# Kernel optimization log

Measured on AMD Instinct MI355X. Metric: run time of the kernel, lower is better.

The kernel has to match this reference:

```python
import jax, jax.numpy as jnp
import numpy as np
from math import sqrt

V, D, H, HD, L, F, P, NL = 32000, 768, 12, 64, 12, 3072, 2048, 2
B, S = 8, 1024
EPS = 1e-5


def setup_inputs() -> dict:
    key = jax.random.key(0)
    ks = jax.random.split(key, 12)
    n = lambda k, sh: (jax.random.normal(k, sh, jnp.float32) * 0.02)
    return {
        'tokens': jax.random.randint(ks[0], (B, S), 0, V, dtype=jnp.int32),
        'tok_emb': n(ks[1], (V, D)),
        'pos_emb': n(ks[2], (P, D)),
        'emb_ln_s': jnp.ones((D,), jnp.float32), 'emb_ln_b': jnp.zeros((D,), jnp.float32),
        'Wq': n(ks[3], (L, H, D, HD)), 'bq': jnp.zeros((L, H, HD), jnp.float32),
        'Wk': n(ks[4], (L, H, D, HD)), 'bk': jnp.zeros((L, H, HD), jnp.float32),
        'Wv': n(ks[5], (L, H, D, HD)), 'bv': jnp.zeros((L, H, HD), jnp.float32),
        'Wo': n(ks[6], (L, D, D)), 'bo': jnp.zeros((L, D), jnp.float32),
        'ln1_s': jnp.ones((L, D), jnp.float32), 'ln1_b': jnp.zeros((L, D), jnp.float32),
        'ln2_s': jnp.ones((L, D), jnp.float32), 'ln2_b': jnp.zeros((L, D), jnp.float32),
        'W1': n(ks[7], (L, D, F)), 'b1': jnp.zeros((L, F), jnp.float32),
        'W2': n(ks[8], (L, F, D)), 'b2': jnp.zeros((L, D), jnp.float32),
        'Wc': n(ks[9], (D, NL)), 'bc': jnp.zeros((NL,), jnp.float32),
    }


def _ln(x, s, b):
    m = jnp.mean(x, -1, keepdims=True)
    v = jnp.mean((x - m) ** 2, -1, keepdims=True)
    return (x - m) * jax.lax.rsqrt(v + EPS) * s + b


def reference(tokens, tok_emb, pos_emb, emb_ln_s, emb_ln_b,
              Wq, bq, Wk, bk, Wv, bv, Wo, bo,
              ln1_s, ln1_b, ln2_s, ln2_b, W1, b1, W2, b2, Wc, bc):
    b, s = tokens.shape
    # embeddings (dropout is eval-mode identity)
    x = tok_emb[tokens] + pos_emb[:s][None, :, :]          # [b, s, D]
    x = _ln(x, emb_ln_s, emb_ln_b)
    scale = 1.0 / sqrt(HD)
    for l in range(L):
        xn = _ln(x, ln1_s[l], ln1_b[l])
        q = jnp.einsum('bsd,hdk->bhsk', xn, Wq[l]) + bq[l][:, None, :]
        k = jnp.einsum('bsd,hdk->bhsk', xn, Wk[l]) + bk[l][:, None, :]
        v = jnp.einsum('bsd,hdk->bhsk', xn, Wv[l]) + bv[l][:, None, :]
        scores = jnp.einsum('bhsk,bhtk->bhst', q, k) * scale   # [b,H,s,s]
        w = jax.nn.softmax(scores, axis=-1)
        o = jnp.einsum('bhst,bhtk->bhsk', w, v)                # [b,H,s,HD]
        o = o.transpose(0, 2, 1, 3).reshape(b, s, D)           # concat heads
        x = x + o @ Wo[l] + bo[l]
        xn = _ln(x, ln2_s[l], ln2_b[l])
        h = jax.nn.gelu(xn @ W1[l] + b1[l], approximate=False)
        x = x + h @ W2[l] + b2[l]
    # CLS token -> classifier (dropout identity)
    return x[:, 0, :] @ Wc + bc                                # [b, NL]
```

## Files before the change

### kernel.cpp

```cpp
#include <hip/hip_runtime.h>
#include <hip/hip_bf16.h>
#include <math.h>

#define B_   8
#define S_   1024
#define D_   768
#define H_   12
#define HD_  64
#define L_   12
#define F_   3072
#define NTOK 8192

typedef __bf16 bf16x8 __attribute__((ext_vector_type(8)));
typedef float  f32x4  __attribute__((ext_vector_type(4)));
typedef unsigned short u16;

static __device__ __forceinline__ unsigned short f2bf_bits(float f) {
    __hip_bfloat16 h = __float2bfloat16(f);
    return __builtin_bit_cast(unsigned short, h);
}
static __device__ __forceinline__ float bf2f(unsigned short u) {
    unsigned int t = ((unsigned int)u) << 16;
    return __builtin_bit_cast(float, t);
}
static __device__ __forceinline__ void gload16(const void* g, void* l) {
    __builtin_amdgcn_global_load_lds(
        (__attribute__((address_space(1))) void*)g,
        (__attribute__((address_space(3))) void*)l, 16, 0, 0);
}

__global__ __launch_bounds__(256)
void prep_layer_kernel(const float* __restrict__ Wq, const float* __restrict__ Wk,
                       const float* __restrict__ Wv, const float* __restrict__ Wo,
                       const float* __restrict__ W1, const float* __restrict__ W2,
                       int l, __hip_bfloat16* __restrict__ wbuf)
{
    const int id = blockIdx.x;
    const float* src; __hip_bfloat16* dst;
    int R, C, r0, c0;
    if (id < 432) {
        int dtile = id % 12, t = id / 12;
        int which = t / 12, h = t % 12;
        src = (which == 0 ? Wq : which == 1 ? Wk : Wv) + (size_t)(l*12 + h) * 768 * 64;
        dst = wbuf + (size_t)(which*768 + h*64) * 768;
        R = 768; C = 64; r0 = dtile * 64; c0 = 0;
    } else if (id < 576) {
        int t = id - 432;
        src = Wo + (size_t)l * 768 * 768;
        dst = wbuf + 1769472;
        R = 768; C = 768; r0 = (t / 12) * 64; c0 = (t % 12) * 64;
    } else if (id < 1152) {
        int t = id - 576;
        src = W1 + (size_t)l * 768 * 3072;
        dst = wbuf + 2359296;
        R = 768; C = 3072; r0 = (t % 12) * 64; c0 = (t / 12) * 64;
    } else {
        int t = id - 1152;
        src = W2 + (size_t)l * 3072 * 768;
        dst = wbuf + 4718592;
        R = 3072; C = 768; r0 = (t / 12) * 64; c0 = (t % 12) * 64;
    }
    __shared__ u16 T[64][68];
    const int t = threadIdx.x;
    const int row = t >> 2, part = t & 3;
#pragma unroll
    for (int j = 0; j < 4; ++j) {
        const int c4 = (part + j*4) * 4;
        float4 v = *(const float4*)(src + (size_t)(r0 + row) * C + c0 + c4);
        T[c4+0][row] = f2bf_bits(v.x);
        T[c4+1][row] = f2bf_bits(v.y);
        T[c4+2][row] = f2bf_bits(v.z);
        T[c4+3][row] = f2bf_bits(v.w);
    }
    __syncthreads();
    const int c = t >> 2;
    u16* drow = (u16*)dst + (size_t)(c0 + c) * R + r0;
#pragma unroll
    for (int j = 0; j < 4; ++j) {
        const int r4 = (part + j*4) * 4;
        ushort4 pk = *(const ushort4*)&T[c][r4];
        *(ushort4*)(drow + r4) = pk;
    }
}

__global__ __launch_bounds__(256)
void prep_bqkv_kernel(const float* __restrict__ bq, const float* __restrict__ bk,
                      const float* __restrict__ bv, float* __restrict__ bqkv)
{
    int i = blockIdx.x * 256 + threadIdx.x;
    int l = i / 2304, c = i % 2304;
    int which = c / 768, hk = c % 768;
    const float* src = which == 0 ? bq : which == 1 ? bk : bv;
    bqkv[i] = src[l*768 + hk];
}

__global__ __launch_bounds__(256)
void embed_ln_kernel(const int* __restrict__ tokens, const float* __restrict__ tok_emb,
                     const float* __restrict__ pos_emb, const float* __restrict__ gam,
                     const float* __restrict__ bet, float* __restrict__ x)
{
    const int row  = blockIdx.x*4 + (threadIdx.x >> 6);
    const int lane = threadIdx.x & 63;
    const int s    = row & (S_-1);
    const int tok  = tokens[row];
    const float* te = tok_emb + (size_t)tok * D_;
    const float* pe = pos_emb + (size_t)s   * D_;
    float v[12]; float s1 = 0.f, s2 = 0.f;
#pragma unroll
    for (int c = 0; c < 3; ++c) {
        const int base = c*256 + lane*4;
        float4 a = *(const float4*)(te + base);
        float4 p = *(const float4*)(pe + base);
        float t0 = a.x+p.x, t1 = a.y+p.y, t2 = a.z+p.z, t3 = a.w+p.w;
        v[c*4+0]=t0; v[c*4+1]=t1; v[c*4+2]=t2; v[c*4+3]=t3;
        s1 += t0+t1+t2+t3;
        s2 += t0*t0 + t1*t1 + t2*t2 + t3*t3;
    }
#pragma unroll
    for (int off = 32; off > 0; off >>= 1) { s1 += __shfl_xor(s1, off); s2 += __shfl_xor(s2, off); }
    const float mean = s1 * (1.f/768.f);
    const float rstd = rsqrtf(s2*(1.f/768.f) - mean*mean + 1e-5f);
    float* xr = x + (size_t)row * D_;
#pragma unroll
    for (int c = 0; c < 3; ++c) {
        const int base = c*256 + lane*4;
        float4 g = *(const float4*)(gam + base);
        float4 bb = *(const float4*)(bet + base);
        float4 o;
        o.x = (v[c*4+0]-mean)*rstd*g.x + bb.x;
        o.y = (v[c*4+1]-mean)*rstd*g.y + bb.y;
        o.z = (v[c*4+2]-mean)*rstd*g.z + bb.z;
        o.w = (v[c*4+3]-mean)*rstd*g.w + bb.w;
        *(float4*)(xr + base) = o;
    }
}

__global__ __launch_bounds__(256)
void ln_kernel(const float* __restrict__ xin, const float* __restrict__ gam,
               const float* __restrict__ bet, __hip_bfloat16* __restrict__ out)
{
    const int row  = blockIdx.x*4 + (threadIdx.x >> 6);
    const int lane = threadIdx.x & 63;
    const float* xr = xin + (size_t)row * D_;
    float v[12]; float s1 = 0.f, s2 = 0.f;
#pragma unroll
    for (int c = 0; c < 3; ++c) {
        float4 t = *(const float4*)(xr + c*256 + lane*4);
        v[c*4+0]=t.x; v[c*4+1]=t.y; v[c*4+2]=t.z; v[c*4+3]=t.w;
        s1 += t.x+t.y+t.z+t.w;
        s2 += t.x*t.x + t.y*t.y + t.z*t.z + t.w*t.w;
    }
#pragma unroll
    for (int off = 32; off > 0; off >>= 1) { s1 += __shfl_xor(s1, off); s2 += __shfl_xor(s2, off); }
    const float mean = s1 * (1.f/768.f);
    const float rstd = rsqrtf(s2*(1.f/768.f) - mean*mean + 1e-5f);
    unsigned short* op = (unsigned short*)out + (size_t)row * D_;
#pragma unroll
    for (int c = 0; c < 3; ++c) {
        const int base = c*256 + lane*4;
        float4 g = *(const float4*)(gam + base);
        float4 bb = *(const float4*)(bet + base);
        ushort4 pk;
        pk.x = f2bf_bits((v[c*4+0]-mean)*rstd*g.x + bb.x);
        pk.y = f2bf_bits((v[c*4+1]-mean)*rstd*g.y + bb.y);
        pk.z = f2bf_bits((v[c*4+2]-mean)*rstd*g.z + bb.z);
        pk.w = f2bf_bits((v[c*4+3]-mean)*rstd*g.w + bb.w);
        *(ushort4*)(op + base) = pk;
    }
}

template<int EPI>
__global__ __launch_bounds__(256)
void gemm128_kernel(const __hip_bfloat16* __restrict__ A,
                    const __hip_bfloat16* __restrict__ Bt,
                    const float* __restrict__ bias,
                    __hip_bfloat16* __restrict__ outb,
                    __hip_bfloat16* __restrict__ outv,
                    int N, int K, int nTiles)
{
    __shared__ __align__(16) char smem[32768];
    char* const As0 = smem;
    char* const As1 = smem + 8192;
    char* const Bs0 = smem + 16384;
    char* const Bs1 = smem + 24576;

    const int tid  = threadIdx.x;
    const int lane = tid & 63;
    const int wid  = tid >> 6;

    const int nwg   = gridDim.x;
    const int chunk = nwg >> 3;
    const int bid   = blockIdx.x;
    const int swz   = (bid & 7) * chunk + (bid >> 3);
    const int m0 = (swz / nTiles) * 128;
    const int n0 = (swz % nTiles) * 128;

    const int l4 = lane >> 2;
    const int sswz = ((lane & 3) ^ ((l4 >> 1) & 3)) * 8;
    const __hip_bfloat16* aSrc = A  + (size_t)(m0 + wid*32 + l4) * K + sswz;
    const __hip_bfloat16* bSrc = Bt + (size_t)(n0 + wid*32 + l4) * K + sswz;
    const int sOff = wid*2048 + lane*16;

    f32x4 acc[4][4] = {};
    const int wm = wid >> 1, wn = wid & 1;
    const int cl = lane & 15, hi = lane >> 4;

    int aoff[4], boff[4];
#pragma unroll
    for (int m = 0; m < 4; ++m) {
        const int row = wm*64 + m*16 + cl;
        aoff[m] = row*64 + ((hi ^ ((row >> 1) & 3)) << 4);
    }
#pragma unroll
    for (int n = 0; n < 4; ++n) {
        const int row = wn*64 + n*16 + cl;
        boff[n] = row*64 + ((hi ^ ((row >> 1) & 3)) << 4);
    }

#pragma unroll
    for (int i = 0; i < 2; ++i) {
        gload16(aSrc + (size_t)i*16*K, As0 + sOff + i*1024);
        gload16(bSrc + (size_t)i*16*K, Bs0 + sOff + i*1024);
    }

    int buf = 0;
    for (int kt = 0; kt < K; kt += 32, buf ^= 1) {
        __syncthreads();
        if (kt + 32 < K) {
            char* an = buf ? As0 : As1;
            char* bn = buf ? Bs0 : Bs1;
#pragma unroll
            for (int i = 0; i < 2; ++i) {
                gload16(aSrc + kt + 32 + (size_t)i*16*K, an + sOff + i*1024);
                gload16(bSrc + kt + 32 + (size_t)i*16*K, bn + sOff + i*1024);
            }
        }
        const char* ac = buf ? As1 : As0;
        const char* bc = buf ? Bs1 : Bs0;

        bf16x8 af[4], bfr[4];
#pragma unroll
        for (int m = 0; m < 4; ++m) af[m]  = *(const bf16x8*)(ac + aoff[m]);
#pragma unroll
        for (int n = 0; n < 4; ++n) bfr[n] = *(const bf16x8*)(bc + boff[n]);
#pragma unroll
        for (int m = 0; m < 4; ++m)
#pragma unroll
            for (int n = 0; n < 4; ++n)
                acc[m][n] = __builtin_amdgcn_mfma_f32_16x16x32_bf16(af[m], bfr[n], acc[m][n], 0, 0, 0);
    }

    __syncthreads();

    const bool vpath = (EPI == 0) && (n0 >= 1536);

    if (!vpath) {
#pragma unroll
        for (int n = 0; n < 4; ++n) {
            const int col2 = wn*64 + n*16 + cl;
            const float bv = bias[n0 + col2];
#pragma unroll
            for (int m = 0; m < 4; ++m) {
#pragma unroll
                for (int i = 0; i < 4; ++i) {
                    const int row = wm*64 + m*16 + hi*4 + i;
                    float v = acc[m][n][i] + bv;
                    if constexpr (EPI == 1) {
                        const float y = 0.7978845608f * (v + 0.044715f*v*v*v);
                        const float e = __expf(-2.0f * fabsf(y));
                        const float th = (1.0f - e) / (1.0f + e);
                        v = 0.5f * v * (1.0f + copysignf(th, y));
                    }
                    *(u16*)(smem + row*256 + ((((col2 >> 3) ^ (row & 15))) << 4)
                                 + ((col2 & 7) << 1)) = f2bf_bits(v);
                }
            }
        }
        __syncthreads();
        const int strideN = (EPI == 0) ? 1536 : N;
        const int r  = tid >> 1;
        const int cb = tid & 1;
        char* dst = (char*)outb + ((size_t)(m0 + r) * strideN + n0) * 2;
#pragma unroll
        for (int j = 0; j < 8; ++j) {
            const int ch = cb + j*2;
            float4 vv = *(const float4*)(smem + r*256 + ((ch ^ (r & 15)) << 4));
            *(float4*)(dst + ch*16) = vv;
        }
    } else {
#pragma unroll
        for (int n = 0; n < 4; ++n) {
            const int hdl = wn*64 + n*16 + cl;
            const float bv = bias[n0 + hdl];
#pragma unroll
            for (int m = 0; m < 4; ++m) {
                const int sl = wm*64 + m*16 + hi*4;
                ushort4 pk;
                pk.x = f2bf_bits(acc[m][n][0] + bv);
                pk.y = f2bf_bits(acc[m][n][1] + bv);
                pk.z = f2bf_bits(acc[m][n][2] + bv);
                pk.w = f2bf_bits(acc[m][n][3] + bv);
                *(ushort4*)(smem + hdl*256 + ((((sl >> 3) ^ (hdl & 15))) << 4) + (sl & 7)*2) = pk;
            }
        }
        __syncthreads();
        const int hdl2 = tid >> 1;
        const int sh   = (tid & 1) * 64;
        const int hdg  = (n0 - 1536) + hdl2;
        const int bb   = m0 >> 10;
        u16* dst = (u16*)outv + ((size_t)(bb*768) + hdg)*1024 + (m0 & 1023) + sh;
#pragma unroll
        for (int j = 0; j < 8; ++j) {
            const int slot = ((sh >> 3) + j) ^ (hdl2 & 15);
            *(float4*)((char*)dst + j*16) = *(const float4*)(smem + hdl2*256 + (slot << 4));
        }
    }
}

__global__ __launch_bounds__(256)
void gemm_res_kernel(const __hip_bfloat16* __restrict__ A,
                     const __hip_bfloat16* __restrict__ Bt,
                     const float* __restrict__ bias,
                     float* __restrict__ outf,
                     int N, int K, int nTiles)
{
    __shared__ __align__(16) char smem[49152];
    char* const As0 = smem;
    char* const As1 = smem + 8192;
    char* const Bs0 = smem + 16384;
    char* const Bs1 = smem + 32768;

    const int tid  = threadIdx.x;
    const int lane = tid & 63;
    const int wid  = tid >> 6;

    const int nwg   = gridDim.x;
    const int chunk = nwg >> 3;
    const int bid   = blockIdx.x;
    const int swz   = (bid & 7) * chunk + (bid >> 3);
    const int m0 = (swz / nTiles) * 64;
    const int n0 = (swz % nTiles) * 128;

    const int lrow = lane >> 3;
    const int scol = ((lane & 7) ^ lrow) * 8;
    const __hip_bfloat16* aSrc = A  + (size_t)(m0 + wid*16 + lrow) * K + scol;
    const __hip_bfloat16* bSrc = Bt + (size_t)(n0 + wid*32 + lrow) * K + scol;
    const int aOff = wid*2048 + lane*16;
    const int bOff = wid*4096 + lane*16;

    f32x4 acc[2][4] = {};
    const int wm = wid >> 1, wn = wid & 1;
    const int cl = lane & 15, hi = lane >> 4;

#pragma unroll
    for (int i = 0; i < 2; ++i)
        gload16(aSrc + (size_t)i*8*K, As0 + aOff + i*1024);
#pragma unroll
    for (int i = 0; i < 4; ++i)
        gload16(bSrc + (size_t)i*8*K, Bs0 + bOff + i*1024);

    int buf = 0;
    for (int kt = 0; kt < K; kt += 64, buf ^= 1) {
        __syncthreads();
        if (kt + 64 < K) {
            char* an = buf ? As0 : As1;
            char* bn = buf ? Bs0 : Bs1;
#pragma unroll
            for (int i = 0; i < 2; ++i)
                gload16(aSrc + kt + 64 + (size_t)i*8*K, an + aOff + i*1024);
#pragma unroll
            for (int i = 0; i < 4; ++i)
                gload16(bSrc + kt + 64 + (size_t)i*8*K, bn + bOff + i*1024);
        }
        const char* ac = buf ? As1 : As0;
        const char* bc = buf ? Bs1 : Bs0;

#pragma unroll
        for (int kk = 0; kk < 2; ++kk) {
            bf16x8 af[2], bfr[4];
#pragma unroll
            for (int m = 0; m < 2; ++m) {
                int row  = wm*32 + m*16 + cl;
                int slot = ((kk<<2) + hi) ^ (row & 7);
                af[m] = *(const bf16x8*)(ac + row*128 + slot*16);
            }
#pragma unroll
            for (int n = 0; n < 4; ++n) {
                int row  = wn*64 + n*16 + cl;
                int slot = ((kk<<2) + hi) ^ (row & 7);
                bfr[n] = *(const bf16x8*)(bc + row*128 + slot*16);
            }
#pragma unroll
            for (int m = 0; m < 2; ++m)
#pragma unroll
                for (int n = 0; n < 4; ++n)
                    acc[m][n] = __builtin_amdgcn_mfma_f32_16x16x32_bf16(af[m], bfr[n], acc[m][n], 0, 0, 0);
        }
    }

    __syncthreads();

#pragma unroll
    for (int n = 0; n < 4; ++n) {
        const int col = wn*64 + n*16 + cl;
        const float bv = bias[n0 + col];
#pragma unroll
        for (int m = 0; m < 2; ++m) {
#pragma unroll
            for (int i = 0; i < 4; ++i) {
                const int row = wm*32 + m*16 + hi*4 + i;
                *(float*)(smem + row*512 + ((((col >> 2) ^ (row & 31))) << 4)
                               + ((col & 3) << 2)) = acc[m][n][i] + bv;
            }
        }
    }
    __syncthreads();
    const int r = tid >> 2;
    const int part = tid & 3;
    float* drow = outf + (size_t)(m0 + r) * N + n0;
#pragma unroll
    for (int j = 0; j < 8; ++j) {
        const int ch = part + j*4;
        f32x4 vv = *(const f32x4*)(smem + r*512 + ((ch ^ (r & 31)) << 4));
        float* dp = drow + ch*4;
        f32x4 g = *(const f32x4*)dp;
        g += vv;
        *(f32x4*)dp = g;
    }
}

__global__ __launch_bounds__(512)
void attn_kernel(const __hip_bfloat16* __restrict__ qkb, const __hip_bfloat16* __restrict__ vtb,
                 __hip_bfloat16* __restrict__ attno)
{
    __shared__ __align__(16) char Ks[2][8192];
    __shared__ __align__(16) char Vs[2][8192];
    __shared__ __align__(16) char Ps[16384];

    const u16* qk = (const u16*)qkb;
    const u16* vt = (const u16*)vtb;
    const int nwg = gridDim.x, bid = blockIdx.x, chunk = nwg >> 3;
    const int swz = (bid & 7) * chunk + (bid >> 3);
    const int bh = swz >> 3, qb = swz & 7;
    const int b = bh / H_, h = bh % H_;
    const int tid = threadIdx.x;
    const int lane = tid & 63, wid = tid >> 6;
    const int cl = lane & 15, hi = lane >> 4;
    const size_t browq = (size_t)(b*S_ + qb*128);

    bf16x8 qf[2];
    {
        const u16* qp = qk + (browq + wid*16 + cl)*1536 + h*64;
        qf[0] = *(const bf16x8*)(qp + hi*8);
        qf[1] = *(const bf16x8*)(qp + 32 + hi*8);
    }

    const int lrow = lane >> 3;
    const int scol = ((lane & 7) ^ lrow) * 8;
    const u16* kbase = qk + ((size_t)b*S_ + wid*8 + lrow)*1536 + 768 + h*64 + scol;
    const u16* vbase = vt + (((size_t)(b*H_ + h))*64 + wid*8 + lrow)*1024 + scol;
    const int ldst = wid*1024 + lane*16;

    f32x4 acc_o[4] = {};
    float m_run = -1e30f;
    float l_part[4] = {0.f, 0.f, 0.f, 0.f};
    char* pbase = Ps + wid*2048;

    {
        gload16(kbase, Ks[0] + ldst);
        gload16(vbase, Vs[0] + ldst);
    }

    for (int t = 0; t < 16; ++t) {
        __syncthreads();
        if (t < 15) {
            const int nb = (t+1) & 1;
            gload16(kbase + (size_t)(t+1)*64*1536, Ks[nb] + ldst);
            gload16(vbase + (t+1)*64,              Vs[nb] + ldst);
        }
        const char* ks = Ks[t & 1];
        const char* vs = Vs[t & 1];

        f32x4 sc[4] = {};
#pragma unroll
        for (int kk = 0; kk < 2; ++kk) {
            bf16x8 kf[4];
#pragma unroll
            for (int n = 0; n < 4; ++n) {
                const int row = n*16 + cl;
                kf[n] = *(const bf16x8*)(ks + row*128 + (((kk*4 + hi) ^ (cl & 7)) << 4));
            }
#pragma unroll
            for (int n = 0; n < 4; ++n)
                sc[n] = __builtin_amdgcn_mfma_f32_16x16x32_bf16(qf[kk], kf[n], sc[n], 0, 0, 0);
        }

#pragma unroll
        for (int n = 0; n < 4; ++n)
#pragma unroll
            for (int i = 0; i < 4; ++i)
                sc[n][i] *= 0.125f;

        float gmax = sc[0][0];
#pragma unroll
        for (int n = 0; n < 4; ++n)
#pragma unroll
            for (int i = 0; i < 4; ++i)
                gmax = fmaxf(gmax, sc[n][i]);
        gmax = fmaxf(gmax, __shfl_xor(gmax, 1));
        gmax = fmaxf(gmax, __shfl_xor(gmax, 2));
        gmax = fmaxf(gmax, __shfl_xor(gmax, 4));
        gmax = fmaxf(gmax, __shfl_xor(gmax, 8));
        if (gmax > m_run + 4.0f) {
            const float corr = __expf(m_run - gmax);
            m_run = gmax;
#pragma unroll
            for (int i = 0; i < 4; ++i) l_part[i] *= corr;
#pragma unroll
            for (int nd = 0; nd < 4; ++nd)
#pragma unroll
                for (int i = 0; i < 4; ++i)
                    acc_o[nd][i] *= corr;
        }

#pragma unroll
        for (int n = 0; n < 4; ++n) {
#pragma unroll
            for (int i = 0; i < 4; ++i) {
                const float e = __expf(sc[n][i] - m_run);
                l_part[i] += e;
                const int q = hi*4 + i;
                const int slot = (n*2 + (cl >> 3)) ^ (q & 7);
                *(u16*)(pbase + q*128 + slot*16 + (cl & 7)*2) = f2bf_bits(e);
            }
        }

        asm volatile("s_waitcnt lgkmcnt(0)" ::: "memory");
        __builtin_amdgcn_sched_barrier(0);

#pragma unroll
        for (int kk = 0; kk < 2; ++kk) {
            const bf16x8 pf = *(const bf16x8*)(pbase + cl*128 + (((kk*4 + hi) ^ (cl & 7)) << 4));
            bf16x8 vf[4];
#pragma unroll
            for (int nd = 0; nd < 4; ++nd) {
                const int d = nd*16 + cl;
                vf[nd] = *(const bf16x8*)(vs + d*128 + (((kk*4 + hi) ^ (d & 7)) << 4));
            }
#pragma unroll
            for (int nd = 0; nd < 4; ++nd)
                acc_o[nd] = __builtin_amdgcn_mfma_f32_16x16x32_bf16(pf, vf[nd], acc_o[nd], 0, 0, 0);
        }
    }

    u16* op = (u16*)attno;
#pragma unroll
    for (int i = 0; i < 4; ++i) {
        float l = l_part[i];
        l += __shfl_xor(l, 1);
        l += __shfl_xor(l, 2);
        l += __shfl_xor(l, 4);
        l += __shfl_xor(l, 8);
        const float inv = 1.f / l;
        const size_t row = browq + wid*16 + hi*4 + i;
#pragma unroll
        for (int nd = 0; nd < 4; ++nd)
            op[row*768 + h*64 + nd*16 + cl] = f2bf_bits(acc_o[nd][i] * inv);
    }
}

__global__ __launch_bounds__(256)
void cls_kernel(const float* __restrict__ x, const float* __restrict__ Wc,
                const float* __restrict__ bc, float* __restrict__ out)
{
    const int b = blockIdx.x;
    const float* xr = x + (size_t)b * S_ * D_;
    float a0 = 0.f, a1 = 0.f;
    for (int d = threadIdx.x; d < 768; d += 256) {
        float xv = xr[d];
        a0 += xv * Wc[d*2+0];
        a1 += xv * Wc[d*2+1];
    }
#pragma unroll
    for (int off = 32; off > 0; off >>= 1) { a0 += __shfl_xor(a0, off); a1 += __shfl_xor(a1, off); }
    __shared__ float r0[4], r1[4];
    const int w = threadIdx.x >> 6;
    if ((threadIdx.x & 63) == 0) { r0[w] = a0; r1[w] = a1; }
    __syncthreads();
    if (threadIdx.x == 0) {
        out[b*2+0] = r0[0]+r0[1]+r0[2]+r0[3] + bc[0];
        out[b*2+1] = r1[0]+r1[1]+r1[2]+r1[3] + bc[1];
    }
}

extern "C" void kernel_launch(void* const* d_in, const int* in_sizes, int n_in,
                              void* d_out, int out_size, void* d_ws, size_t ws_size,
                              hipStream_t stream)
{
    const int*   tokens  = (const int*)  d_in[0];
    const float* tok_emb = (const float*)d_in[1];
    const float* pos_emb = (const float*)d_in[2];
    const float* e_s     = (const float*)d_in[3];
    const float* e_b     = (const float*)d_in[4];
    const float* Wq      = (const float*)d_in[5];
    const float* bq      = (const float*)d_in[6];
    const float* Wk      = (const float*)d_in[7];
    const float* bk      = (const float*)d_in[8];
    const float* Wv      = (const float*)d_in[9];
    const float* bv      = (const float*)d_in[10];
    const float* Wo      = (const float*)d_in[11];
    const float* bo      = (const float*)d_in[12];
    const float* l1s     = (const float*)d_in[13];
    const float* l1b     = (const float*)d_in[14];
    const float* l2s     = (const float*)d_in[15];
    const float* l2b     = (const float*)d_in[16];
    const float* W1      = (const float*)d_in[17];
    const float* b1      = (const float*)d_in[18];
    const float* W2      = (const float*)d_in[19];
    const float* b2      = (const float*)d_in[20];
    const float* Wc      = (const float*)d_in[21];
    const float* bc      = (const float*)d_in[22];
    (void)in_sizes; (void)n_in; (void)out_size;

    if (ws_size < 102346752) return;

    char* ws = (char*)d_ws;
    __hip_bfloat16* wbuf = (__hip_bfloat16*)(ws + 0);
    float*          bqkv = (float*)(ws + 14155776);
    float*          x    = (float*)(ws + 14266368);
    __hip_bfloat16* xn   = (__hip_bfloat16*)(ws + 39432192);
    __hip_bfloat16* qk   = (__hip_bfloat16*)(ws + 52015104);
    __hip_bfloat16* vT   = (__hip_bfloat16*)(ws + 77180928);
    __hip_bfloat16* att  = (__hip_bfloat16*)(ws + 89763840);
    __hip_bfloat16* hbuf = qk;

    __hip_bfloat16* wqkv_t = wbuf;
    __hip_bfloat16* wo_t   = wbuf + 1769472;
    __hip_bfloat16* w1_t   = wbuf + 2359296;
    __hip_bfloat16* w2_t   = wbuf + 4718592;

    prep_bqkv_kernel<<<108, 256, 0, stream>>>(bq, bk, bv, bqkv);
    embed_ln_kernel<<<2048, 256, 0, stream>>>(tokens, tok_emb, pos_emb, e_s, e_b, x);

    for (int l = 0; l < L_; ++l) {
        prep_layer_kernel<<<1728, 256, 0, stream>>>(Wq, Wk, Wv, Wo, W1, W2, l, wbuf);
        ln_kernel<<<2048, 256, 0, stream>>>(x, l1s + l*768, l1b + l*768, xn);
        gemm128_kernel<0><<<1152, 256, 0, stream>>>(xn, wqkv_t, bqkv + l*2304, qk, vT, 2304, 768, 18);
        attn_kernel<<<768, 512, 0, stream>>>(qk, vT, att);
        gemm_res_kernel<<<768, 256, 0, stream>>>(att, wo_t, bo + l*768, x, 768, 768, 6);
        ln_kernel<<<2048, 256, 0, stream>>>(x, l2s + l*768, l2b + l*768, xn);
        gemm128_kernel<1><<<1536, 256, 0, stream>>>(xn, w1_t, b1 + l*3072, hbuf, nullptr, 3072, 768, 24);
        gemm_res_kernel<<<768, 256, 0, stream>>>(hbuf, w2_t, b2 + l*768, x, 768, 3072, 6);
    }
    cls_kernel<<<8, 256, 0, stream>>>(x, Wc, bc, (float*)d_out);
}
```

Baseline: 3.065 ms.

## Use 256x128 tiles with 512 threads and explicit waitcnt pipelining in GEMMs

The QKV and FFN1 GEMMs move from 128x128 tiles with 256 threads to 256x128 tiles with 512 threads. Both GEMM kernels replace the syncthreads double buffer with an explicit prefetch two stages ahead, using vmcnt/lgkmcnt waits, raw barriers and MFMA priority hints, so global loads overlap compute. The non-V epilogue now writes bf16 scalars straight to global memory instead of staging them through shared memory, which may reduce store coalescing. Larger tiles add LDS and register pressure per workgroup.

```diff
diff --git a/kernel.cpp b/kernel.cpp
--- a/kernel.cpp
+++ b/kernel.cpp
@@ -170,19 +170,19 @@
 }
 
 template<int EPI>
-__global__ __launch_bounds__(256)
-void gemm128_kernel(const __hip_bfloat16* __restrict__ A,
+__global__ __launch_bounds__(512, 2)
+void gemm256_kernel(const __hip_bfloat16* __restrict__ A,
                     const __hip_bfloat16* __restrict__ Bt,
                     const float* __restrict__ bias,
                     __hip_bfloat16* __restrict__ outb,
                     __hip_bfloat16* __restrict__ outv,
                     int N, int K, int nTiles)
 {
-    __shared__ __align__(16) char smem[32768];
+    __shared__ __align__(16) char smem[49152];
     char* const As0 = smem;
-    char* const As1 = smem + 8192;
-    char* const Bs0 = smem + 16384;
-    char* const Bs1 = smem + 24576;
+    char* const As1 = smem + 16384;
+    char* const Bs0 = smem + 32768;
+    char* const Bs1 = smem + 40960;
 
     const int tid  = threadIdx.x;
     const int lane = tid & 63;
@@ -192,14 +192,14 @@
     const int chunk = nwg >> 3;
     const int bid   = blockIdx.x;
     const int swz   = (bid & 7) * chunk + (bid >> 3);
-    const int m0 = (swz / nTiles) * 128;
+    const int m0 = (swz / nTiles) * 256;
     const int n0 = (swz % nTiles) * 128;
 
     const int l4 = lane >> 2;
     const int sswz = ((lane & 3) ^ ((l4 >> 1) & 3)) * 8;
-    const __hip_bfloat16* aSrc = A  + (size_t)(m0 + wid*32 + l4) * K + sswz;
-    const __hip_bfloat16* bSrc = Bt + (size_t)(n0 + wid*32 + l4) * K + sswz;
-    const int sOff = wid*2048 + lane*16;
+    const __hip_bfloat16* aSrc = A  + (size_t)(m0 + wid*16 + l4) * K + sswz;
+    const __hip_bfloat16* bSrc = Bt + (size_t)(n0 + wid*16 + l4) * K + sswz;
+    const int sOff = wid*1024 + lane*16;
 
     f32x4 acc[4][4] = {};
     const int wm = wid >> 1, wn = wid & 1;
@@ -217,53 +217,56 @@
         boff[n] = row*64 + ((hi ^ ((row >> 1) & 3)) << 4);
     }
 
-#pragma unroll
-    for (int i = 0; i < 2; ++i) {
-        gload16(aSrc + (size_t)i*16*K, As0 + sOff + i*1024);
-        gload16(bSrc + (size_t)i*16*K, Bs0 + sOff + i*1024);
-    }
-
-    int buf = 0;
-    for (int kt = 0; kt < K; kt += 32, buf ^= 1) {
-        __syncthreads();
-        if (kt + 32 < K) {
-            char* an = buf ? As0 : As1;
-            char* bn = buf ? Bs0 : Bs1;
-#pragma unroll
-            for (int i = 0; i < 2; ++i) {
-                gload16(aSrc + kt + 32 + (size_t)i*16*K, an + sOff + i*1024);
-                gload16(bSrc + kt + 32 + (size_t)i*16*K, bn + sOff + i*1024);
-            }
-        }
-        const char* ac = buf ? As1 : As0;
-        const char* bc = buf ? Bs1 : Bs0;
-
+    auto STAGE = [&](char* aBuf, char* bBuf, int kt) {
+        gload16(aSrc + kt,                  aBuf + sOff);
+        gload16(aSrc + kt + (size_t)128*K,  aBuf + 8192 + sOff);
+        gload16(bSrc + kt,                  bBuf + sOff);
+    };
+
+    const int NT = K >> 5;
+    STAGE(As0, Bs0, 0);
+    STAGE(As1, Bs1, 32);
+
+    for (int t = 0; t < NT; ++t) {
+        if (t < NT - 1) asm volatile("s_waitcnt vmcnt(3)" ::: "memory");
+        else            asm volatile("s_waitcnt vmcnt(0)" ::: "memory");
+        __builtin_amdgcn_s_barrier();
+
+        char* const ac = (t & 1) ? As1 : As0;
+        char* const bc = (t & 1) ? Bs1 : Bs0;
         bf16x8 af[4], bfr[4];
 #pragma unroll
         for (int m = 0; m < 4; ++m) af[m]  = *(const bf16x8*)(ac + aoff[m]);
 #pragma unroll
         for (int n = 0; n < 4; ++n) bfr[n] = *(const bf16x8*)(bc + boff[n]);
+        asm volatile("s_waitcnt lgkmcnt(0)" ::: "memory");
+        __builtin_amdgcn_sched_barrier(0);
+        __builtin_amdgcn_s_barrier();
+
+        if (t + 2 < NT) STAGE(ac, bc, (t + 2) << 5);
+
+        __builtin_amdgcn_s_setprio(1);
 #pragma unroll
         for (int m = 0; m < 4; ++m)
 #pragma unroll
             for (int n = 0; n < 4; ++n)
                 acc[m][n] = __builtin_amdgcn_mfma_f32_16x16x32_bf16(af[m], bfr[n], acc[m][n], 0, 0, 0);
-    }
-
-    __syncthreads();
+        __builtin_amdgcn_s_setprio(0);
+    }
 
     const bool vpath = (EPI == 0) && (n0 >= 1536);
 
     if (!vpath) {
+        const int strideN = (EPI == 0) ? 1536 : N;
 #pragma unroll
         for (int n = 0; n < 4; ++n) {
-            const int col2 = wn*64 + n*16 + cl;
-            const float bv = bias[n0 + col2];
+            const int col = n0 + wn*64 + n*16 + cl;
+            const float bv = bias[col];
 #pragma unroll
             for (int m = 0; m < 4; ++m) {
 #pragma unroll
                 for (int i = 0; i < 4; ++i) {
-                    const int row = wm*64 + m*16 + hi*4 + i;
+                    const int row = m0 + wm*64 + m*16 + hi*4 + i;
                     float v = acc[m][n][i] + bv;
                     if constexpr (EPI == 1) {
                         const float y = 0.7978845608f * (v + 0.044715f*v*v*v);
@@ -271,48 +274,45 @@
                         const float th = (1.0f - e) / (1.0f + e);
                         v = 0.5f * v * (1.0f + copysignf(th, y));
                     }
-                    *(u16*)(smem + row*256 + ((((col2 >> 3) ^ (row & 15))) << 4)
-                                 + ((col2 & 7) << 1)) = f2bf_bits(v);
+                    outb[(size_t)row*strideN + col] = __float2bfloat16(v);
                 }
             }
         }
-        __syncthreads();
-        const int strideN = (EPI == 0) ? 1536 : N;
-        const int r  = tid >> 1;
-        const int cb = tid & 1;
-        char* dst = (char*)outb + ((size_t)(m0 + r) * strideN + n0) * 2;
-#pragma unroll
-        for (int j = 0; j < 8; ++j) {
-            const int ch = cb + j*2;
-            float4 vv = *(const float4*)(smem + r*256 + ((ch ^ (r & 15)) << 4));
-            *(float4*)(dst + ch*16) = vv;
-        }
     } else {
-#pragma unroll
-        for (int n = 0; n < 4; ++n) {
-            const int hdl = wn*64 + n*16 + cl;
-            const float bv = bias[n0 + hdl];
-#pragma unroll
-            for (int m = 0; m < 4; ++m) {
-                const int sl = wm*64 + m*16 + hi*4;
-                ushort4 pk;
-                pk.x = f2bf_bits(acc[m][n][0] + bv);
-                pk.y = f2bf_bits(acc[m][n][1] + bv);
-                pk.z = f2bf_bits(acc[m][n][2] + bv);
-                pk.w = f2bf_bits(acc[m][n][3] + bv);
-                *(ushort4*)(smem + hdl*256 + ((((sl >> 3) ^ (hdl & 15))) << 4) + (sl & 7)*2) = pk;
-            }
-        }
-        __syncthreads();
-        const int hdl2 = tid >> 1;
-        const int sh   = (tid & 1) * 64;
-        const int hdg  = (n0 - 1536) + hdl2;
-        const int bb   = m0 >> 10;
-        u16* dst = (u16*)outv + ((size_t)(bb*768) + hdg)*1024 + (m0 & 1023) + sh;
-#pragma unroll
-        for (int j = 0; j < 8; ++j) {
-            const int slot = ((sh >> 3) + j) ^ (hdl2 & 15);
-            *(float4*)((char*)dst + j*16) = *(const float4*)(smem + hdl2*256 + (slot << 4));
+        const int hdbase = n0 - 1536;
+        const int bb = m0 >> 10;
+#pragma unroll
+        for (int half = 0; half < 2; ++half) {
+            __syncthreads();
+            if ((wm >> 1) == half) {
+#pragma unroll
+                for (int n = 0; n < 4; ++n) {
+                    const int hdl = wn*64 + n*16 + cl;
+                    const float bv = bias[n0 + hdl];
+#pragma unroll
+                    for (int m = 0; m < 4; ++m) {
+                        const int sl = (wm & 1)*64 + m*16 + hi*4;
+                        ushort4 pk;
+                        pk.x = f2bf_bits(acc[m][n][0] + bv);
+                        pk.y = f2bf_bits(acc[m][n][1] + bv);
+                        pk.z = f2bf_bits(acc[m][n][2] + bv);
+                        pk.w = f2bf_bits(acc[m][n][3] + bv);
+                        *(ushort4*)(smem + hdl*256 + ((((sl >> 3) ^ (hdl & 15))) << 4)
+                                         + (sl & 7)*2) = pk;
+                    }
+                }
+            }
+            __syncthreads();
+            const int hdl2 = tid >> 2;
+            const int q4   = tid & 3;
+            u16* dst = (u16*)outv + ((size_t)(bb*768) + hdbase + hdl2)*1024
+                                  + (m0 & 1023) + half*128;
+#pragma unroll
+            for (int j = 0; j < 4; ++j) {
+                const int ch = q4*4 + j;
+                const int slot = ch ^ (hdl2 & 15);
+                *(float4*)((char*)dst + ch*16) = *(const float4*)(smem + hdl2*256 + (slot << 4));
+            }
         }
     }
 }
@@ -352,50 +352,57 @@
     const int wm = wid >> 1, wn = wid & 1;
     const int cl = lane & 15, hi = lane >> 4;
 
-#pragma unroll
-    for (int i = 0; i < 2; ++i)
-        gload16(aSrc + (size_t)i*8*K, As0 + aOff + i*1024);
-#pragma unroll
-    for (int i = 0; i < 4; ++i)
-        gload16(bSrc + (size_t)i*8*K, Bs0 + bOff + i*1024);
-
-    int buf = 0;
-    for (int kt = 0; kt < K; kt += 64, buf ^= 1) {
-        __syncthreads();
-        if (kt + 64 < K) {
-            char* an = buf ? As0 : As1;
-            char* bn = buf ? Bs0 : Bs1;
-#pragma unroll
-            for (int i = 0; i < 2; ++i)
-                gload16(aSrc + kt + 64 + (size_t)i*8*K, an + aOff + i*1024);
-#pragma unroll
-            for (int i = 0; i < 4; ++i)
-                gload16(bSrc + kt + 64 + (size_t)i*8*K, bn + bOff + i*1024);
-        }
-        const char* ac = buf ? As1 : As0;
-        const char* bc = buf ? Bs1 : Bs0;
-
+    auto STAGE = [&](char* aBuf, char* bBuf, int kt) {
+#pragma unroll
+        for (int i = 0; i < 2; ++i)
+            gload16(aSrc + kt + (size_t)i*8*K, aBuf + aOff + i*1024);
+#pragma unroll
+        for (int i = 0; i < 4; ++i)
+            gload16(bSrc + kt + (size_t)i*8*K, bBuf + bOff + i*1024);
+    };
+
+    const int NT = K >> 6;
+    STAGE(As0, Bs0, 0);
+    STAGE(As1, Bs1, 64);
+
+    for (int t = 0; t < NT; ++t) {
+        if (t < NT - 1) asm volatile("s_waitcnt vmcnt(6)" ::: "memory");
+        else            asm volatile("s_waitcnt vmcnt(0)" ::: "memory");
+        __builtin_amdgcn_s_barrier();
+
+        char* const ac = (t & 1) ? As1 : As0;
+        char* const bc = (t & 1) ? Bs1 : Bs0;
+        bf16x8 af[2][2], bfr[2][4];
 #pragma unroll
         for (int kk = 0; kk < 2; ++kk) {
-            bf16x8 af[2], bfr[4];
 #pragma unroll
             for (int m = 0; m < 2; ++m) {
-                int row  = wm*32 + m*16 + cl;
-                int slot = ((kk<<2) + hi) ^ (row & 7);
-                af[m] = *(const bf16x8*)(ac + row*128 + slot*16);
+                const int row  = wm*32 + m*16 + cl;
+                const int slot = ((kk<<2) + hi) ^ (row & 7);
+                af[kk][m] = *(const bf16x8*)(ac + row*128 + slot*16);
             }
 #pragma unroll
             for (int n = 0; n < 4; ++n) {
-                int row  = wn*64 + n*16 + cl;
-                int slot = ((kk<<2) + hi) ^ (row & 7);
-                bfr[n] = *(const bf16x8*)(bc + row*128 + slot*16);
-            }
+                const int row  = wn*64 + n*16 + cl;
+                const int slot = ((kk<<2) + hi) ^ (row & 7);
+                bfr[kk][n] = *(const bf16x8*)(bc + row*128 + slot*16);
+            }
+        }
+        asm volatile("s_waitcnt lgkmcnt(0)" ::: "memory");
+        __builtin_amdgcn_sched_barrier(0);
+        __builtin_amdgcn_s_barrier();
+
+        if (t + 2 < NT) STAGE(ac, bc, (t + 2) << 6);
+
+        __builtin_amdgcn_s_setprio(1);
+#pragma unroll
+        for (int kk = 0; kk < 2; ++kk)
 #pragma unroll
             for (int m = 0; m < 2; ++m)
 #pragma unroll
                 for (int n = 0; n < 4; ++n)
-                    acc[m][n] = __builtin_amdgcn_mfma_f32_16x16x32_bf16(af[m], bfr[n], acc[m][n], 0, 0, 0);
-        }
+                    acc[m][n] = __builtin_amdgcn_mfma_f32_16x16x32_bf16(af[kk][m], bfr[kk][n], acc[m][n], 0, 0, 0);
+        __builtin_amdgcn_s_setprio(0);
     }
 
     __syncthreads();
@@ -645,11 +652,11 @@
     for (int l = 0; l < L_; ++l) {
         prep_layer_kernel<<<1728, 256, 0, stream>>>(Wq, Wk, Wv, Wo, W1, W2, l, wbuf);
         ln_kernel<<<2048, 256, 0, stream>>>(x, l1s + l*768, l1b + l*768, xn);
-        gemm128_kernel<0><<<1152, 256, 0, stream>>>(xn, wqkv_t, bqkv + l*2304, qk, vT, 2304, 768, 18);
+        gemm256_kernel<0><<<576, 512, 0, stream>>>(xn, wqkv_t, bqkv + l*2304, qk, vT, 2304, 768, 18);
         attn_kernel<<<768, 512, 0, stream>>>(qk, vT, att);
         gemm_res_kernel<<<768, 256, 0, stream>>>(att, wo_t, bo + l*768, x, 768, 768, 6);
         ln_kernel<<<2048, 256, 0, stream>>>(x, l2s + l*768, l2b + l*768, xn);
-        gemm128_kernel<1><<<1536, 256, 0, stream>>>(xn, w1_t, b1 + l*3072, hbuf, nullptr, 3072, 768, 24);
+        gemm256_kernel<1><<<768, 512, 0, stream>>>(xn, w1_t, b1 + l*3072, hbuf, nullptr, 3072, 768, 24);
         gemm_res_kernel<<<768, 256, 0, stream>>>(hbuf, w2_t, b2 + l*768, x, 768, 3072, 6);
     }
     cls_kernel<<<8, 256, 0, stream>>>(x, Wc, bc, (float*)d_out);
```

Result: faster. 2.949 ms, median of 2 (-3.8%).
